# Kernel optimization log

Measured on AMD Instinct MI355X. Metric: run time of the kernel, lower is better.

The kernel has to match this reference:

```python
import jax, jax.numpy as jnp
import numpy as np

N_NODES = 100000
N_EDGES = 1000000
D_IN = 256
D_OUT = 64


def setup_inputs() -> dict:
    key = jax.random.key(0)
    k1, k2, k3, k4, k5, k6 = jax.random.split(key, 6)
    x = jax.random.normal(k1, (N_NODES, D_IN), dtype=jnp.float32)
    # Xavier-style uniform init: stdv = 1/sqrt(output_dim)
    stdv = 1.0 / np.sqrt(D_OUT)
    weight = jax.random.uniform(k2, (D_IN, D_OUT), dtype=jnp.float32, minval=-stdv, maxval=stdv)
    adj_vals = jax.random.uniform(k3, (N_EDGES,), dtype=jnp.float32)
    prelu_a = jnp.full((1,), 0.25, dtype=jnp.float32)  # nn.PReLU default
    row = jax.random.randint(k4, (N_EDGES,), 0, N_NODES, dtype=jnp.int32)
    col = jax.random.randint(k5, (N_EDGES,), 0, N_NODES, dtype=jnp.int32)
    return {"x": x, "weight": weight, "adj_vals": adj_vals, "prelu_a": prelu_a,
            "row": row, "col": col}


def reference(x, weight, adj_vals, prelu_a, row, col):
    # dense GEMM: [N, D_in] @ [D_in, D_out]
    hidden = x @ weight  # gc_drop=0 -> identity dropout
    # sparse adj spmm: out[i] = sum_{e: row[e]=i} adj_vals[e] * hidden[col[e]]
    msg = adj_vals[:, None] * hidden[col]  # [E, D_out]
    agg = jax.ops.segment_sum(msg, row, num_segments=N_NODES)  # [N, D_out]
    # PReLU with single shared slope
    out = jnp.where(agg > 0, agg, prelu_a * agg)
    return out
```

## Files before the change

### kernel.cpp

```cpp
#include <hip/hip_runtime.h>

#define N_NODES 100000
#define N_EDGES 1000000
#define D_IN    256
#define D_OUT   64

#define BKT_SHIFT   5
#define NODES_PER_BKT 32
#define N_BKT       3125
#define BKT_CAP     512
#define EPB         8192
#define BIN_BLOCKS  123
#define GEMM_BLOCKS 782
#define NUM_TILES   6250
#define AGG_BLOCKS  391

typedef __attribute__((ext_vector_type(8))) short short8;
typedef __attribute__((ext_vector_type(4))) float f32x4;

__device__ __forceinline__ unsigned short f2bf(float f) {
    unsigned int u = __float_as_uint(f);
    u = (u + 0x7fffu + ((u >> 16) & 1u)) >> 16;
    return (unsigned short)u;
}

__device__ __forceinline__ void mfma_store_tile(
    const short8 afrag[8], const unsigned short wT[64][272],
    unsigned short* __restrict__ hiddenBf, int r0, int n16, int quad)
{
    f32x4 acc[4] = {{0.f,0.f,0.f,0.f},{0.f,0.f,0.f,0.f},
                    {0.f,0.f,0.f,0.f},{0.f,0.f,0.f,0.f}};
#pragma unroll
    for (int ct = 0; ct < 4; ++ct) {
#pragma unroll
        for (int kk = 0; kk < 8; ++kk) {
            short8 b = *(const short8*)&wT[ct * 16 + n16][kk * 32 + quad * 8];
            acc[ct] = __builtin_amdgcn_mfma_f32_16x16x32_bf16(
                afrag[kk], b, acc[ct], 0, 0, 0);
        }
    }
#pragma unroll
    for (int ct = 0; ct < 4; ++ct)
#pragma unroll
        for (int reg = 0; reg < 4; ++reg)
            hiddenBf[(size_t)(r0 + quad * 4 + reg) * D_OUT + ct * 16 + n16]
                = f2bf(acc[ct][reg]);
}

__global__ __launch_bounds__(256, 2) void gemm_bin_kernel(
    const float* __restrict__ x, const float* __restrict__ w,
    unsigned short* __restrict__ hiddenBf,
    const int* __restrict__ row, const int* __restrict__ col,
    const float* __restrict__ adj, int* __restrict__ gCursor,
    int2* __restrict__ edges)
{
    const int t = threadIdx.x;

    if (blockIdx.x < BIN_BLOCKS) {
        __shared__ int cnt[N_BKT];
        __shared__ int cbase[N_BKT];
        __shared__ int cur[N_BKT];

        const int e0 = blockIdx.x * EPB;

        for (int i = t; i < N_BKT; i += 256) cnt[i] = 0;
        __syncthreads();

        int rreg[32];
#pragma unroll
        for (int u = 0; u < 32; ++u) {
            int e = e0 + t + u * 256;
            rreg[u] = (e < N_EDGES) ? row[e] : -1;
        }
#pragma unroll
        for (int u = 0; u < 32; ++u)
            if (rreg[u] >= 0) atomicAdd(&cnt[rreg[u] >> BKT_SHIFT], 1);
        __syncthreads();

        for (int i = t; i < N_BKT; i += 256) {
            int c = cnt[i];
            cbase[i] = c ? atomicAdd(&gCursor[i], c) : 0;
            cur[i] = 0;
        }
        __syncthreads();

#pragma unroll
        for (int u0 = 0; u0 < 32; u0 += 8) {
            int   cc[8]; float vv[8];
#pragma unroll
            for (int u = 0; u < 8; ++u) {
                int e = e0 + t + (u0 + u) * 256;
                if (rreg[u0 + u] >= 0) { cc[u] = col[e]; vv[u] = adj[e]; }
                else                   { cc[u] = 0;      vv[u] = 0.f;    }
            }
#pragma unroll
            for (int u = 0; u < 8; ++u) {
                int r = rreg[u0 + u];
                if (r >= 0) {
                    int b = r >> BKT_SHIFT;
                    int off = cbase[b] + atomicAdd(&cur[b], 1);
                    if (off < BKT_CAP) {
                        edges[b * BKT_CAP + off] =
                            make_int2(((r & (NODES_PER_BKT - 1)) << 17) | cc[u],
                                      __float_as_int(vv[u]));
                    }
                }
            }
        }
        return;
    }

    __shared__ unsigned short wT[64][272];

    for (int i = 0; i < 64; ++i) {
        int idx = t + i * 256;
        int k = idx >> 6, n = idx & 63;
        wT[n][k] = f2bf(w[idx]);
    }
    __syncthreads();

    const int lane = t & 63;
    const int wid  = t >> 6;
    const int n16  = lane & 15;
    const int quad = lane >> 4;

    const int waveGid = (blockIdx.x - BIN_BLOCKS) * 4 + wid;
    const int t0 = waveGid * 2;
    if (t0 >= NUM_TILES) return;

    float4 lo[8], hi[8];
    short8 afrag[8];

    {
        const float* xrow = x + (size_t)(t0 * 16 + n16) * D_IN + quad * 8;
#pragma unroll
        for (int kk = 0; kk < 8; ++kk) {
            lo[kk] = *(const float4*)(xrow + kk * 32);
            hi[kk] = *(const float4*)(xrow + kk * 32 + 4);
        }
    }
#pragma unroll
    for (int kk = 0; kk < 8; ++kk) {
        short8 a;
        a[0] = (short)f2bf(lo[kk].x); a[1] = (short)f2bf(lo[kk].y);
        a[2] = (short)f2bf(lo[kk].z); a[3] = (short)f2bf(lo[kk].w);
        a[4] = (short)f2bf(hi[kk].x); a[5] = (short)f2bf(hi[kk].y);
        a[6] = (short)f2bf(hi[kk].z); a[7] = (short)f2bf(hi[kk].w);
        afrag[kk] = a;
    }

    const int t1 = t0 + 1;
    const bool have1 = t1 < NUM_TILES;
    if (have1) {
        const float* xrow = x + (size_t)(t1 * 16 + n16) * D_IN + quad * 8;
#pragma unroll
        for (int kk = 0; kk < 8; ++kk) {
            lo[kk] = *(const float4*)(xrow + kk * 32);
            hi[kk] = *(const float4*)(xrow + kk * 32 + 4);
        }
    }

    mfma_store_tile(afrag, wT, hiddenBf, t0 * 16, n16, quad);

    if (have1) {
#pragma unroll
        for (int kk = 0; kk < 8; ++kk) {
            short8 a;
            a[0] = (short)f2bf(lo[kk].x); a[1] = (short)f2bf(lo[kk].y);
            a[2] = (short)f2bf(lo[kk].z); a[3] = (short)f2bf(lo[kk].w);
            a[4] = (short)f2bf(hi[kk].x); a[5] = (short)f2bf(hi[kk].y);
            a[6] = (short)f2bf(hi[kk].z); a[7] = (short)f2bf(hi[kk].w);
            afrag[kk] = a;
        }
        mfma_store_tile(afrag, wT, hiddenBf, t1 * 16, n16, quad);
    }
}

__global__ __launch_bounds__(512, 2) void bucket_agg_kernel(
    const unsigned short* __restrict__ hiddenBf,
    const int2* __restrict__ edges, const int* __restrict__ gCursor,
    const float* __restrict__ prelu_a, float* __restrict__ out)
{
    __shared__ float acc[8][NODES_PER_BKT * D_OUT];

    const int t      = threadIdx.x;
    const int lane   = t & 63;
    const int wid    = t >> 6;
    const int bucket = blockIdx.x * 8 + wid;
    if (bucket >= N_BKT) return;

    float* A = acc[wid];

    float4* A4 = (float4*)A;
#pragma unroll
    for (int i = 0; i < 8; ++i)
        A4[lane + i * 64] = make_float4(0.f, 0.f, 0.f, 0.f);

    const int base = bucket * BKT_CAP;
    int size = gCursor[bucket];
    if (size > BKT_CAP) size = BKT_CAP;

    for (int i0 = 0; i0 < size; i0 += 64) {
        int take = size - i0;
        if (take > 64) take = 64;
        int2 rec = make_int2(0, 0);
        if (lane < take) rec = edges[base + i0 + lane];

        int j = 0;
        for (; j + 8 <= take; j += 8) {
            int nl[8]; int c[8]; float v[8]; float h[8];
#pragma unroll
            for (int u = 0; u < 8; ++u) {
                int rx = __builtin_amdgcn_readlane(rec.x, j + u);
                nl[u] = (unsigned)rx >> 17;
                c[u]  = rx & 0x1FFFF;
                v[u]  = __int_as_float(__builtin_amdgcn_readlane(rec.y, j + u));
            }
#pragma unroll
            for (int u = 0; u < 8; ++u)
                h[u] = __uint_as_float(
                    (unsigned)hiddenBf[(size_t)c[u] * D_OUT + lane] << 16);
#pragma unroll
            for (int u = 0; u < 8; ++u)
                A[nl[u] * D_OUT + lane] += v[u] * h[u];
        }
        for (; j < take; ++j) {
            int rx  = __builtin_amdgcn_readlane(rec.x, j);
            float v = __int_as_float(__builtin_amdgcn_readlane(rec.y, j));
            float h = __uint_as_float(
                (unsigned)hiddenBf[(size_t)(rx & 0x1FFFF) * D_OUT + lane] << 16);
            A[((unsigned)rx >> 17) * D_OUT + lane] += v * h;
        }
    }

    const float a = prelu_a[0];
    const int node0 = bucket * NODES_PER_BKT;
#pragma unroll
    for (int i = 0; i < NODES_PER_BKT; ++i) {
        float s = A[i * D_OUT + lane];
        out[(size_t)(node0 + i) * D_OUT + lane] = s > 0.f ? s : a * s;
    }
}

extern "C" void kernel_launch(void* const* d_in, const int* in_sizes, int n_in,
                              void* d_out, int out_size, void* d_ws, size_t ws_size,
                              hipStream_t stream)
{
    const float* x       = (const float*)d_in[0];
    const float* w       = (const float*)d_in[1];
    const float* adj     = (const float*)d_in[2];
    const float* prelu_a = (const float*)d_in[3];
    const int*   row     = (const int*)d_in[4];
    const int*   col     = (const int*)d_in[5];
    float* out = (float*)d_out;

    char* ws = (char*)d_ws;
    unsigned short* hiddenBf = (unsigned short*)(ws);
    int2*  edges    = (int2*)        (ws + 12800000);
    int*   gCursor  = (int*)         (ws + 25600000);

    hipMemsetAsync(gCursor, 0, N_BKT * sizeof(int), stream);

    gemm_bin_kernel<<<BIN_BLOCKS + GEMM_BLOCKS, 256, 0, stream>>>(
        x, w, hiddenBf, row, col, adj, gCursor, edges);

    bucket_agg_kernel<<<AGG_BLOCKS, 512, 0, stream>>>(
        hiddenBf, edges, gCursor, prelu_a, out);
}
```

Baseline: 243.0 us.

## Split fused gemm/bin kernel, use smaller binning blocks, deepen gather unroll

Splits the combined GEMM+binning launch into separate bin and GEMM kernels. The bin kernel gets 4x more blocks, each handling fewer edges (2048 instead of 8192), which cuts per-thread register use and raises parallelism. The aggregation loop gains a 16-wide unrolled gather to keep more hidden-row loads in flight. The costs are an extra kernel launch, more global atomics on bucket cursors (more blocks each reserving space per bucket), and the loss of GEMM/bin overlap within one launch.

```diff
diff --git a/kernel.cpp b/kernel.cpp
--- a/kernel.cpp
+++ b/kernel.cpp
@@ -9,8 +9,9 @@
 #define NODES_PER_BKT 32
 #define N_BKT       3125
 #define BKT_CAP     512
-#define EPB         8192
-#define BIN_BLOCKS  123
+
+#define EPB         2048
+#define BIN_BLOCKS  489
 #define GEMM_BLOCKS 782
 #define NUM_TILES   6250
 #define AGG_BLOCKS  391
@@ -47,68 +48,66 @@
                 = f2bf(acc[ct][reg]);
 }
 
-__global__ __launch_bounds__(256, 2) void gemm_bin_kernel(
-    const float* __restrict__ x, const float* __restrict__ w,
-    unsigned short* __restrict__ hiddenBf,
+__global__ __launch_bounds__(256, 2) void bin_kernel(
     const int* __restrict__ row, const int* __restrict__ col,
     const float* __restrict__ adj, int* __restrict__ gCursor,
     int2* __restrict__ edges)
 {
+    __shared__ int cnt[N_BKT];
+    __shared__ int cbase[N_BKT];
+    __shared__ int cur[N_BKT];
+
+    const int t  = threadIdx.x;
+    const int e0 = blockIdx.x * EPB;
+
+    for (int i = t; i < N_BKT; i += 256) cnt[i] = 0;
+    __syncthreads();
+
+    int rreg[8];
+#pragma unroll
+    for (int u = 0; u < 8; ++u) {
+        int e = e0 + t + u * 256;
+        rreg[u] = (e < N_EDGES) ? row[e] : -1;
+    }
+#pragma unroll
+    for (int u = 0; u < 8; ++u)
+        if (rreg[u] >= 0) atomicAdd(&cnt[rreg[u] >> BKT_SHIFT], 1);
+    __syncthreads();
+
+    for (int i = t; i < N_BKT; i += 256) {
+        int c = cnt[i];
+        cbase[i] = c ? atomicAdd(&gCursor[i], c) : 0;
+        cur[i] = 0;
+    }
+    __syncthreads();
+
+    int cc[8]; float vv[8];
+#pragma unroll
+    for (int u = 0; u < 8; ++u) {
+        int e = e0 + t + u * 256;
+        if (rreg[u] >= 0) { cc[u] = col[e]; vv[u] = adj[e]; }
+        else              { cc[u] = 0;      vv[u] = 0.f;    }
+    }
+#pragma unroll
+    for (int u = 0; u < 8; ++u) {
+        int r = rreg[u];
+        if (r >= 0) {
+            int b = r >> BKT_SHIFT;
+            int off = cbase[b] + atomicAdd(&cur[b], 1);
+            if (off < BKT_CAP) {
+                edges[b * BKT_CAP + off] =
+                    make_int2(((r & (NODES_PER_BKT - 1)) << 17) | cc[u],
+                              __float_as_int(vv[u]));
+            }
+        }
+    }
+}
+
+__global__ __launch_bounds__(256, 2) void gemm_kernel(
+    const float* __restrict__ x, const float* __restrict__ w,
+    unsigned short* __restrict__ hiddenBf)
+{
     const int t = threadIdx.x;
-
-    if (blockIdx.x < BIN_BLOCKS) {
-        __shared__ int cnt[N_BKT];
-        __shared__ int cbase[N_BKT];
-        __shared__ int cur[N_BKT];
-
-        const int e0 = blockIdx.x * EPB;
-
-        for (int i = t; i < N_BKT; i += 256) cnt[i] = 0;
-        __syncthreads();
-
-        int rreg[32];
-#pragma unroll
-        for (int u = 0; u < 32; ++u) {
-            int e = e0 + t + u * 256;
-            rreg[u] = (e < N_EDGES) ? row[e] : -1;
-        }
-#pragma unroll
-        for (int u = 0; u < 32; ++u)
-            if (rreg[u] >= 0) atomicAdd(&cnt[rreg[u] >> BKT_SHIFT], 1);
-        __syncthreads();
-
-        for (int i = t; i < N_BKT; i += 256) {
-            int c = cnt[i];
-            cbase[i] = c ? atomicAdd(&gCursor[i], c) : 0;
-            cur[i] = 0;
-        }
-        __syncthreads();
-
-#pragma unroll
-        for (int u0 = 0; u0 < 32; u0 += 8) {
-            int   cc[8]; float vv[8];
-#pragma unroll
-            for (int u = 0; u < 8; ++u) {
-                int e = e0 + t + (u0 + u) * 256;
-                if (rreg[u0 + u] >= 0) { cc[u] = col[e]; vv[u] = adj[e]; }
-                else                   { cc[u] = 0;      vv[u] = 0.f;    }
-            }
-#pragma unroll
-            for (int u = 0; u < 8; ++u) {
-                int r = rreg[u0 + u];
-                if (r >= 0) {
-                    int b = r >> BKT_SHIFT;
-                    int off = cbase[b] + atomicAdd(&cur[b], 1);
-                    if (off < BKT_CAP) {
-                        edges[b * BKT_CAP + off] =
-                            make_int2(((r & (NODES_PER_BKT - 1)) << 17) | cc[u],
-                                      __float_as_int(vv[u]));
-                    }
-                }
-            }
-        }
-        return;
-    }
 
     __shared__ unsigned short wT[64][272];
 
@@ -124,7 +123,7 @@
     const int n16  = lane & 15;
     const int quad = lane >> 4;
 
-    const int waveGid = (blockIdx.x - BIN_BLOCKS) * 4 + wid;
+    const int waveGid = blockIdx.x * 4 + wid;
     const int t0 = waveGid * 2;
     if (t0 >= NUM_TILES) return;
 
@@ -207,6 +206,23 @@
         if (lane < take) rec = edges[base + i0 + lane];
 
         int j = 0;
+        for (; j + 16 <= take; j += 16) {
+            int nl[16]; int c[16]; float v[16]; float h[16];
+#pragma unroll
+            for (int u = 0; u < 16; ++u) {
+                int rx = __builtin_amdgcn_readlane(rec.x, j + u);
+                nl[u] = (unsigned)rx >> 17;
+                c[u]  = rx & 0x1FFFF;
+                v[u]  = __int_as_float(__builtin_amdgcn_readlane(rec.y, j + u));
+            }
+#pragma unroll
+            for (int u = 0; u < 16; ++u)
+                h[u] = __uint_as_float(
+                    (unsigned)hiddenBf[(size_t)c[u] * D_OUT + lane] << 16);
+#pragma unroll
+            for (int u = 0; u < 16; ++u)
+                A[nl[u] * D_OUT + lane] += v[u] * h[u];
+        }
         for (; j + 8 <= take; j += 8) {
             int nl[8]; int c[8]; float v[8]; float h[8];
 #pragma unroll
@@ -261,8 +277,9 @@
 
     hipMemsetAsync(gCursor, 0, N_BKT * sizeof(int), stream);
 
-    gemm_bin_kernel<<<BIN_BLOCKS + GEMM_BLOCKS, 256, 0, stream>>>(
-        x, w, hiddenBf, row, col, adj, gCursor, edges);
+    bin_kernel<<<BIN_BLOCKS, 256, 0, stream>>>(row, col, adj, gCursor, edges);
+
+    gemm_kernel<<<GEMM_BLOCKS, 256, 0, stream>>>(x, w, hiddenBf);
 
     bucket_agg_kernel<<<AGG_BLOCKS, 512, 0, stream>>>(
         hiddenBf, edges, gCursor, prelu_a, out);
```

Result: slower. 251.9 us (+3.7%).
